# Optimization experiments

Measured on AMD Instinct MI355X. Metric: run time of the kernel, lower is better.

Reference implementation:

```python
import jax, jax.numpy as jnp
import numpy as np

B, S, D, H = 2, 2048, 2048, 16
HD = D // H


def setup_inputs() -> dict:
    key = jax.random.key(0)
    ks = jax.random.split(key, 9)
    scale = 0.02
    return {
        "x": jax.random.normal(ks[0], (B, S, D), dtype=jnp.float32),
        "wq_w": jax.random.normal(ks[1], (D, D), dtype=jnp.float32) * scale,
        "wq_b": jnp.zeros((D,), dtype=jnp.float32),
        "wk_w": jax.random.normal(ks[2], (D, D), dtype=jnp.float32) * scale,
        "wk_b": jnp.zeros((D,), dtype=jnp.float32),
        "wv_w": jax.random.normal(ks[3], (D, D), dtype=jnp.float32) * scale,
        "wv_b": jnp.zeros((D,), dtype=jnp.float32),
        "wo_w": jax.random.normal(ks[4], (D, D), dtype=jnp.float32) * scale,
        "wo_b": jnp.zeros((D,), dtype=jnp.float32),
    }


def reference(x, wq_w, wq_b, wk_w, wk_b, wv_w, wv_b, wo_w, wo_b):
    # torch Linear: y = x @ W.T + b
    q = x @ wq_w.T + wq_b  # [B,S,D]
    k = x @ wk_w.T + wk_b
    v = x @ wv_w.T + wv_b
    # [B,S,D] -> [B,H,S,HD]
    q = q.reshape(B, S, H, HD).transpose(0, 2, 1, 3)
    k = k.reshape(B, S, H, HD).transpose(0, 2, 1, 3)
    v = v.reshape(B, S, H, HD).transpose(0, 2, 1, 3)
    # scores [B,H,S,S], scaled by sqrt(d_dim) as in the original (not head_dim)
    scores = jnp.einsum("bhid,bhjd->bhij", q, k) / np.float32(np.sqrt(D))
    # faithful reproduction of the module's triu/transpose masking:
    m = jnp.swapaxes(jnp.triu(scores), -2, -1)  # lower-tri, zeros elsewhere
    p = jax.nn.softmax(m, axis=-2)              # softmax over dim=-2, zeros included
    a = jnp.swapaxes(jnp.triu(p), -2, -1)       # [B,H,S,S]
    attn = jnp.einsum("bhij,bhjd->bhid", a, v)  # [B,H,S,HD]
    concat = attn.transpose(0, 2, 1, 3).reshape(B, S, D)
    return concat @ wo_w.T + wo_b
```

## Files before the change

kernel.cpp:

```cpp
#include <hip/hip_runtime.h>

#define BB 2
#define SS 2048
#define DD 2048
#define HH 16
#define HDIM 128
#define MTOK (BB*SS)
#define BHH (BB*HH)
#define NCHUNK 16
#define QKN (2*DD)

typedef __attribute__((ext_vector_type(8))) __bf16 bf16x8;
typedef __attribute__((ext_vector_type(4))) float f32x4;
typedef __attribute__((ext_vector_type(8))) int i32x8;

__device__ __forceinline__ unsigned short f2bf(float f) {
  unsigned u = __float_as_uint(f);
  u += 0x7FFFu + ((u >> 16) & 1u);
  return (unsigned short)(u >> 16);
}
__device__ __forceinline__ float bf2f(unsigned short s) {
  return __uint_as_float(((unsigned)s) << 16);
}
__device__ __forceinline__ unsigned char f2e4m3(float f) {
  int pk = __builtin_amdgcn_cvt_pk_fp8_f32(f, f, 0, false);
  return (unsigned char)(pk & 0xFF);
}

#define GLOAD_LDS16(src, dst)                                                   \
  __builtin_amdgcn_global_load_lds(                                             \
      (const void __attribute__((address_space(1)))*)(src),                     \
      (void __attribute__((address_space(3)))*)(dst), 16, 0, 0)

__global__ void cvt_x_dual(const float* __restrict__ in,
                           unsigned short* __restrict__ outb,
                           unsigned int* __restrict__ out8, int n4) {
  int i = blockIdx.x * blockDim.x + threadIdx.x;
  if (i < n4) {
    float4 v = ((const float4*)in)[i];
    ushort4 o;
    o.x = f2bf(v.x); o.y = f2bf(v.y); o.z = f2bf(v.z); o.w = f2bf(v.w);
    ((ushort4*)outb)[i] = o;
    int p0 = __builtin_amdgcn_cvt_pk_fp8_f32(v.x, v.y, 0, false);
    int p1 = __builtin_amdgcn_cvt_pk_fp8_f32(v.z, v.w, 0, false);
    out8[i] = (unsigned)(p0 & 0xFFFF) | ((unsigned)(p1 & 0xFFFF) << 16);
  }
}

__global__ void cvt_wqk8(const float* __restrict__ a, const float* __restrict__ b,
                         unsigned int* __restrict__ out) {
  int i = blockIdx.x * blockDim.x + threadIdx.x;
  int sel = i >> 20, r = i & 0xFFFFF;
  const float* src = sel == 0 ? a : b;
  float4 v = ((const float4*)src)[r];
  int p0 = __builtin_amdgcn_cvt_pk_fp8_f32(v.x, v.y, 0, false);
  int p1 = __builtin_amdgcn_cvt_pk_fp8_f32(v.z, v.w, 0, false);
  out[i] = (unsigned)(p0 & 0xFFFF) | ((unsigned)(p1 & 0xFFFF) << 16);
}

__global__ void cvt_w2bf(const float* __restrict__ a, const float* __restrict__ b,
                         unsigned short* __restrict__ out) {
  int i = blockIdx.x * blockDim.x + threadIdx.x;
  int sel = i >> 20, r = i & 0xFFFFF;
  const float* src = sel == 0 ? a : b;
  float4 v = ((const float4*)src)[r];
  ushort4 o;
  o.x = f2bf(v.x); o.y = f2bf(v.y); o.z = f2bf(v.z); o.w = f2bf(v.w);
  ((ushort4*)out)[i] = o;
}

__global__ void concat2(const float* __restrict__ a, const float* __restrict__ b,
                        float* __restrict__ out) {
  int i = blockIdx.x * blockDim.x + threadIdx.x;
  if (i < DD) { out[i] = a[i]; out[DD + i] = b[i]; }
}

template <bool OUT_BF16>
__global__ __launch_bounds__(256, 2) void gemm_bt(
    const __bf16* __restrict__ A, const __bf16* __restrict__ W,
    const float* __restrict__ bias, void* __restrict__ Cout,
    int M, int N, int K) {
  __shared__ __bf16 lA[128 * 32];
  __shared__ __bf16 lB[128 * 32];
  const int t = threadIdx.x;
  const int lane = t & 63, wave = t >> 6;
  const int quad = lane >> 4, l16 = lane & 15;
  const int m0 = blockIdx.y * 128, n0 = blockIdx.x * 128;
  const int wm = (wave & 1) * 64, wn = (wave >> 1) * 64;

  f32x4 acc[4][4] = {};

  for (int k0 = 0; k0 < K; k0 += 32) {
#pragma unroll
    for (int c = 0; c < 2; ++c) {
      int lin = c * 256 + t;
      int row = lin >> 2;
      int col = (lin & 3) * 8;
      const __bf16* srcA = A + (size_t)(m0 + row) * K + k0 + col;
      const __bf16* srcB = W + (size_t)(n0 + row) * K + k0 + col;
      GLOAD_LDS16(srcA, &lA[(c * 256 + wave * 64) * 8]);
      GLOAD_LDS16(srcB, &lB[(c * 256 + wave * 64) * 8]);
    }
    __syncthreads();
    bf16x8 af[4], bfr[4];
#pragma unroll
    for (int mt = 0; mt < 4; ++mt)
      af[mt] = *(const bf16x8*)&lA[(wm + mt * 16 + l16) * 32 + quad * 8];
#pragma unroll
    for (int nt = 0; nt < 4; ++nt)
      bfr[nt] = *(const bf16x8*)&lB[(wn + nt * 16 + l16) * 32 + quad * 8];
#pragma unroll
    for (int mt = 0; mt < 4; ++mt)
#pragma unroll
      for (int nt = 0; nt < 4; ++nt)
        acc[mt][nt] = __builtin_amdgcn_mfma_f32_16x16x32_bf16(af[mt], bfr[nt],
                                                              acc[mt][nt], 0, 0, 0);
    __syncthreads();
  }

#pragma unroll
  for (int mt = 0; mt < 4; ++mt) {
#pragma unroll
    for (int nt = 0; nt < 4; ++nt) {
      int col = n0 + wn + nt * 16 + l16;
      float bv = bias[col];
#pragma unroll
      for (int r = 0; r < 4; ++r) {
        int row = m0 + wm + mt * 16 + quad * 4 + r;
        float v = acc[mt][nt][r] + bv;
        if constexpr (OUT_BF16)
          ((unsigned short*)Cout)[(size_t)row * N + col] = f2bf(v);
        else
          ((float*)Cout)[(size_t)row * N + col] = v;
      }
    }
  }
}

__global__ __launch_bounds__(256, 2) void gemm_qk_fp8(
    const unsigned char* __restrict__ A8, const unsigned char* __restrict__ W8,
    const float* __restrict__ bias, unsigned char* __restrict__ Cout,
    int M, int N, int K) {
  __shared__ unsigned char lA[128 * 128];
  __shared__ unsigned char lB[128 * 128];
  const int t = threadIdx.x;
  const int lane = t & 63, wave = t >> 6;
  const int quad = lane >> 4, l16 = lane & 15;
  const int m0 = blockIdx.y * 128, n0 = blockIdx.x * 128;
  const int wm = (wave & 1) * 64, wn = (wave >> 1) * 64;

  f32x4 acc[4][4] = {};

  for (int k0 = 0; k0 < K; k0 += 128) {
#pragma unroll
    for (int c = 0; c < 4; ++c) {
      int lin = c * 256 + t;
      int row = lin >> 3;
      int ch = lin & 7;
      const unsigned char* srcA = A8 + (size_t)(m0 + row) * K + k0 + ch * 16;
      const unsigned char* srcB = W8 + (size_t)(n0 + row) * K + k0 + ch * 16;
      GLOAD_LDS16(srcA, &lA[(c * 256 + wave * 64) * 16]);
      GLOAD_LDS16(srcB, &lB[(c * 256 + wave * 64) * 16]);
    }
    __syncthreads();
    i32x8 af[4];
#pragma unroll
    for (int mt = 0; mt < 4; ++mt)
      af[mt] = *(const i32x8*)&lA[(wm + mt * 16 + l16) * 128 + quad * 32];
#pragma unroll
    for (int nt = 0; nt < 4; ++nt) {
      i32x8 bfr = *(const i32x8*)&lB[(wn + nt * 16 + l16) * 128 + quad * 32];
#pragma unroll
      for (int mt = 0; mt < 4; ++mt)
        acc[mt][nt] = __builtin_amdgcn_mfma_scale_f32_16x16x128_f8f6f4(
            af[mt], bfr, acc[mt][nt], 0 , 0 ,
            0, 127 , 0, 127 );
    }
    __syncthreads();
  }

#pragma unroll
  for (int mt = 0; mt < 4; ++mt) {
#pragma unroll
    for (int nt = 0; nt < 4; ++nt) {
      int col = n0 + wn + nt * 16 + l16;
      float bv = bias[col];
#pragma unroll
      for (int r = 0; r < 4; ++r) {
        int row = m0 + wm + mt * 16 + quad * 4 + r;
        Cout[(size_t)row * N + col] = f2e4m3(acc[mt][nt][r] + bv);
      }
    }
  }
}

__global__ __launch_bounds__(256, 2) void qk_rowsum8(
    const unsigned char* __restrict__ q8, const unsigned char* __restrict__ k8,
    float* __restrict__ denom, float* __restrict__ diag) {
  __shared__ unsigned char lK[4 * 128 * 32];
  const int t = threadIdx.x;
  const int lane = t & 63, wave = t >> 6;
  const int quad = lane >> 4, l16 = lane & 15;
  const int bh = blockIdx.y;
  const int b = bh >> 4, h = bh & 15;
  const float scale = 0.02209708691207961f;

#pragma unroll
  for (int sub = 0; sub < 2; ++sub) {
    const int tile = (sub == 0) ? (int)blockIdx.x : 31 - (int)blockIdx.x;
    const int i0 = tile * 64;
    const int rowg = i0 + wave * 16;

    long long af[4];
    const unsigned char* qbase =
        q8 + (size_t)(b * SS + rowg + l16) * QKN + h * HDIM;
#pragma unroll
    for (int ks = 0; ks < 4; ++ks)
      af[ks] = *(const long long*)(qbase + ks * 32 + quad * 8);

    float rowsum[4] = {0.f, 0.f, 0.f, 0.f};
    float diagv[4] = {0.f, 0.f, 0.f, 0.f};

    for (int j0 = i0 & ~127; j0 < SS; j0 += 128) {
#pragma unroll
      for (int c = 0; c < 4; ++c) {
        int L = c * 256 + t;
        int ks = L >> 8;
        int rem = L & 255;
        int row = rem >> 1;
        int c2 = rem & 1;
        const unsigned char* src =
            k8 + (size_t)(b * SS + j0 + row) * QKN + h * HDIM + ks * 32 + c2 * 16;
        GLOAD_LDS16(src, &lK[(c * 256 + wave * 64) * 16]);
      }
      __syncthreads();
#pragma unroll
      for (int nt = 0; nt < 8; ++nt) {
        f32x4 acc = {0.f, 0.f, 0.f, 0.f};
#pragma unroll
        for (int ks = 0; ks < 4; ++ks) {
          long long bfr =
              *(const long long*)&lK[ks * 4096 + (nt * 16 + l16) * 32 + quad * 8];
          acc = __builtin_amdgcn_mfma_f32_16x16x32_fp8_fp8(af[ks], bfr, acc, 0, 0, 0);
        }
        int colg = j0 + nt * 16 + l16;
#pragma unroll
        for (int r = 0; r < 4; ++r) {
          int rg = rowg + quad * 4 + r;
          if (colg >= rg) {
            float e = __expf(acc[r] * scale);
            rowsum[r] += e;
            if (colg == rg) diagv[r] = e;
          }
        }
      }
      __syncthreads();
    }

#pragma unroll
    for (int r = 0; r < 4; ++r) {
      float s = rowsum[r], d = diagv[r];
#pragma unroll
      for (int off = 1; off < 16; off <<= 1) {
        s += __shfl_xor(s, off, 64);
        d += __shfl_xor(d, off, 64);
      }
      if (l16 == 0) {
        int rg = rowg + quad * 4 + r;
        denom[bh * SS + rg] = (float)rg + s;
        diag[bh * SS + rg] = d;
      }
    }
  }
}

__global__ void scan_pass1(const __bf16* __restrict__ v0,
                           float* __restrict__ csum) {
  int blk = blockIdx.x;
  int bh = blk >> 4, c = blk & 15;
  int b = bh >> 4, h = bh & 15;
  int t = threadIdx.x;
  int rs = t >> 4, dg = t & 15;
  const unsigned short* base = (const unsigned short*)v0 +
      (size_t)(b * SS + c * 128 + rs * 8) * DD + h * HDIM + dg * 8;
  float s[8] = {0.f, 0.f, 0.f, 0.f, 0.f, 0.f, 0.f, 0.f};
#pragma unroll
  for (int i = 0; i < 8; ++i) {
    uint4 u = *(const uint4*)(base + (size_t)i * DD);
    const unsigned short* us = (const unsigned short*)&u;
#pragma unroll
    for (int j = 0; j < 8; ++j) s[j] += bf2f(us[j]);
  }
  __shared__ float red[16 * 128];
#pragma unroll
  for (int j = 0; j < 8; ++j) red[rs * 128 + dg * 8 + j] = s[j];
  __syncthreads();
  for (int st = 8; st >= 1; st >>= 1) {
    if (rs < st) {
#pragma unroll
      for (int j = 0; j < 8; ++j)
        red[rs * 128 + dg * 8 + j] += red[(rs + st) * 128 + dg * 8 + j];
    }
    __syncthreads();
  }
  if (rs == 0) {
#pragma unroll
    for (int j = 0; j < 8; ++j)
      csum[(size_t)blk * 128 + dg * 8 + j] = red[dg * 8 + j];
  }
}

__global__ void scan_pass2(const __bf16* __restrict__ v0,
                           const float* __restrict__ csum,
                           const float* __restrict__ denom,
                           const float* __restrict__ diag,
                           unsigned short* __restrict__ ctx) {
  int blk = blockIdx.x;
  int bh = blk >> 4, c = blk & 15;
  int b = bh >> 4, h = bh & 15;
  int t = threadIdx.x;
  int rs = t >> 4, dg = t & 15;
  const unsigned short* vbase = (const unsigned short*)v0 +
      (size_t)(b * SS + c * 128 + rs * 8) * DD + h * HDIM + dg * 8;
  float vrow[8][8];
  float ls[8] = {0.f, 0.f, 0.f, 0.f, 0.f, 0.f, 0.f, 0.f};
#pragma unroll
  for (int i = 0; i < 8; ++i) {
    uint4 u = *(const uint4*)(vbase + (size_t)i * DD);
    const unsigned short* us = (const unsigned short*)&u;
#pragma unroll
    for (int j = 0; j < 8; ++j) {
      vrow[i][j] = bf2f(us[j]);
      ls[j] += vrow[i][j];
    }
  }
  __shared__ float red[16 * 128];
#pragma unroll
  for (int j = 0; j < 8; ++j) red[rs * 128 + dg * 8 + j] = ls[j];
  __syncthreads();

  float pre[8] = {0.f, 0.f, 0.f, 0.f, 0.f, 0.f, 0.f, 0.f};
  for (int cc = 0; cc < c; ++cc) {
    const float* cp = csum + (size_t)(bh * 16 + cc) * 128 + dg * 8;
#pragma unroll
    for (int j = 0; j < 8; ++j) pre[j] += cp[j];
  }
  for (int ss2 = 0; ss2 < rs; ++ss2) {
#pragma unroll
    for (int j = 0; j < 8; ++j) pre[j] += red[ss2 * 128 + dg * 8 + j];
  }

  int row0 = c * 128 + rs * 8;
  unsigned short* obase =
      ctx + (size_t)(b * SS + row0) * DD + h * HDIM + dg * 8;
  const float* dn = denom + bh * SS + row0;
  const float* dgp = diag + bh * SS + row0;
#pragma unroll
  for (int i = 0; i < 8; ++i) {
    float inv = 1.0f / dn[i];
    float dv = dgp[i];
    unsigned short o[8];
#pragma unroll
    for (int j = 0; j < 8; ++j) {
      float val = (pre[j] + dv * vrow[i][j]) * inv;
      o[j] = f2bf(val);
      pre[j] += vrow[i][j];
    }
    *(uint4*)(obase + (size_t)i * DD) = *(const uint4*)o;
  }
}

extern "C" void kernel_launch(void* const* d_in, const int* in_sizes, int n_in,
                              void* d_out, int out_size, void* d_ws, size_t ws_size,
                              hipStream_t stream) {
  (void)in_sizes; (void)n_in; (void)out_size; (void)ws_size;
  const float* x    = (const float*)d_in[0];
  const float* wq_w = (const float*)d_in[1];
  const float* wq_b = (const float*)d_in[2];
  const float* wk_w = (const float*)d_in[3];
  const float* wk_b = (const float*)d_in[4];
  const float* wv_w = (const float*)d_in[5];
  const float* wv_b = (const float*)d_in[6];
  const float* wo_w = (const float*)d_in[7];
  const float* wo_b = (const float*)d_in[8];

  char* ws = (char*)d_ws;
  size_t off = 0;
  auto alloc = [&](size_t bytes) {
    char* p = ws + off;
    off += (bytes + 255) & ~(size_t)255;
    return p;
  };
  unsigned short* xb   = (unsigned short*)alloc((size_t)MTOK * DD * 2);
  unsigned char*  x8   = (unsigned char*)alloc((size_t)MTOK * DD);
  unsigned char*  wqk8 = (unsigned char*)alloc((size_t)2 * DD * DD);
  unsigned short* wvo  = (unsigned short*)alloc((size_t)2 * DD * DD * 2);
  unsigned char*  qk8  = (unsigned char*)alloc((size_t)MTOK * QKN);
  unsigned short* v    = (unsigned short*)alloc((size_t)MTOK * DD * 2);
  unsigned short* ctx  = (unsigned short*)alloc((size_t)MTOK * DD * 2);
  float* biasqk = (float*)alloc((size_t)2 * DD * 4);
  float* denom  = (float*)alloc((size_t)BHH * SS * 4);
  float* diag   = (float*)alloc((size_t)BHH * SS * 4);
  float* csum   = (float*)alloc((size_t)BHH * NCHUNK * 128 * 4);

  {
    int n4 = MTOK * DD / 4;
    cvt_x_dual<<<n4 / 256, 256, 0, stream>>>(x, xb, (unsigned int*)x8, n4);
    cvt_wqk8<<<(2 << 20) / 256, 256, 0, stream>>>(wq_w, wk_w, (unsigned int*)wqk8);
    cvt_w2bf<<<(2 << 20) / 256, 256, 0, stream>>>(wv_w, wo_w, wvo);
    concat2<<<(DD + 255) / 256, 256, 0, stream>>>(wq_b, wk_b, biasqk);
  }

  gemm_qk_fp8<<<dim3(QKN / 128, MTOK / 128), 256, 0, stream>>>(
      x8, wqk8, biasqk, qk8, MTOK, QKN, DD);

  gemm_bt<true><<<dim3(DD / 128, MTOK / 128), 256, 0, stream>>>(
      (const __bf16*)xb, (const __bf16*)wvo, wv_b, v, MTOK, DD, DD);

  qk_rowsum8<<<dim3(16, BHH), 256, 0, stream>>>(
      qk8,
      qk8 + DD,
      denom, diag);

  scan_pass1<<<BHH * NCHUNK, 256, 0, stream>>>((const __bf16*)v, csum);
  scan_pass2<<<BHH * NCHUNK, 256, 0, stream>>>((const __bf16*)v, csum,
                                               denom, diag, ctx);

  gemm_bt<false><<<dim3(DD / 128, MTOK / 128), 256, 0, stream>>>(
      (const __bf16*)ctx, (const __bf16*)(wvo + (size_t)DD * DD), wo_b,
      d_out, MTOK, DD, DD);
}
```

Before: 367.8 us.

## Rework QK rowsum kernel with K=128 MFMA, double buffering, split-K halves, swizzled LDS

The QK row-sum kernel now uses the 16x16x128 scaled FP8 MFMA over 64-row tiles per block, double-buffers the K tiles in LDS, and splits the column range across two blocks. The two partial denominators are written to separate buffers and added in scan_pass2. Causal masking is applied only on the first diagonal tile, and exp is computed with exp2 and a folded constant. Both the QK GEMM and the rowsum kernel use an XOR swizzle on their LDS layouts to reduce bank conflicts. In exchange the kernel uses more LDS and registers, and the launch-bounds occupancy hint is raised.

```diff
diff --git a/kernel.cpp b/kernel.cpp
--- a/kernel.cpp
+++ b/kernel.cpp
@@ -13,6 +13,7 @@
 typedef __attribute__((ext_vector_type(8))) __bf16 bf16x8;
 typedef __attribute__((ext_vector_type(4))) float f32x4;
 typedef __attribute__((ext_vector_type(8))) int i32x8;
+typedef __attribute__((ext_vector_type(4))) int i32x4;
 
 __device__ __forceinline__ unsigned short f2bf(float f) {
   unsigned u = __float_as_uint(f);
@@ -148,6 +149,7 @@
   const int quad = lane >> 4, l16 = lane & 15;
   const int m0 = blockIdx.y * 128, n0 = blockIdx.x * 128;
   const int wm = (wave & 1) * 64, wn = (wave >> 1) * 64;
+  const int p0 = (2 * quad) ^ (l16 & 7);
 
   f32x4 acc[4][4] = {};
 
@@ -157,19 +159,26 @@
       int lin = c * 256 + t;
       int row = lin >> 3;
       int ch = lin & 7;
-      const unsigned char* srcA = A8 + (size_t)(m0 + row) * K + k0 + ch * 16;
-      const unsigned char* srcB = W8 + (size_t)(n0 + row) * K + k0 + ch * 16;
+      int sch = ch ^ (row & 7);
+      const unsigned char* srcA = A8 + (size_t)(m0 + row) * K + k0 + sch * 16;
+      const unsigned char* srcB = W8 + (size_t)(n0 + row) * K + k0 + sch * 16;
       GLOAD_LDS16(srcA, &lA[(c * 256 + wave * 64) * 16]);
       GLOAD_LDS16(srcB, &lB[(c * 256 + wave * 64) * 16]);
     }
     __syncthreads();
     i32x8 af[4];
 #pragma unroll
-    for (int mt = 0; mt < 4; ++mt)
-      af[mt] = *(const i32x8*)&lA[(wm + mt * 16 + l16) * 128 + quad * 32];
+    for (int mt = 0; mt < 4; ++mt) {
+      int ra = (wm + mt * 16 + l16) * 128 + p0 * 16;
+      ((i32x4*)&af[mt])[0] = *(const i32x4*)&lA[ra];
+      ((i32x4*)&af[mt])[1] = *(const i32x4*)&lA[ra ^ 16];
+    }
 #pragma unroll
     for (int nt = 0; nt < 4; ++nt) {
-      i32x8 bfr = *(const i32x8*)&lB[(wn + nt * 16 + l16) * 128 + quad * 32];
+      int rb = (wn + nt * 16 + l16) * 128 + p0 * 16;
+      i32x8 bfr;
+      ((i32x4*)&bfr)[0] = *(const i32x4*)&lB[rb];
+      ((i32x4*)&bfr)[1] = *(const i32x4*)&lB[rb ^ 16];
 #pragma unroll
       for (int mt = 0; mt < 4; ++mt)
         acc[mt][nt] = __builtin_amdgcn_mfma_scale_f32_16x16x128_f8f6f4(
@@ -194,81 +203,151 @@
   }
 }
 
-__global__ __launch_bounds__(256, 2) void qk_rowsum8(
+__global__ __launch_bounds__(256, 4) void qk_rowsum8(
     const unsigned char* __restrict__ q8, const unsigned char* __restrict__ k8,
-    float* __restrict__ denom, float* __restrict__ diag) {
-  __shared__ unsigned char lK[4 * 128 * 32];
+    float* __restrict__ denomA, float* __restrict__ denomB,
+    float* __restrict__ diag) {
+  __shared__ unsigned char lK[2][128 * 128];
+  __shared__ float redS[4][64];
+  __shared__ float redD[4][64];
   const int t = threadIdx.x;
   const int lane = t & 63, wave = t >> 6;
   const int quad = lane >> 4, l16 = lane & 15;
   const int bh = blockIdx.y;
   const int b = bh >> 4, h = bh & 15;
-  const float scale = 0.02209708691207961f;
-
-#pragma unroll
+  const int pair = blockIdx.x >> 1;
+  const int half = blockIdx.x & 1;
+  const float C = 0.03187935771f;
+  const f32x4 fz = {0.f, 0.f, 0.f, 0.f};
+
+  int soff[4];
+#pragma unroll
+  for (int c = 0; c < 4; ++c) {
+    int L = c * 256 + t;
+    int row = L >> 3, p = L & 7;
+    soff[c] = row * QKN + ((p ^ (row & 7)) * 16);
+  }
+  const int p0 = (2 * quad) ^ (l16 & 7);
+  int bo[2];
+#pragma unroll
+  for (int nt = 0; nt < 2; ++nt)
+    bo[nt] = (wave * 32 + nt * 16 + l16) * 128 + p0 * 16;
+
+  const unsigned char* kbase = k8 + (size_t)(b * SS) * QKN + h * HDIM;
+
   for (int sub = 0; sub < 2; ++sub) {
-    const int tile = (sub == 0) ? (int)blockIdx.x : 31 - (int)blockIdx.x;
+    const int tile = (sub == 0) ? pair : 31 - pair;
     const int i0 = tile * 64;
-    const int rowg = i0 + wave * 16;
-
-    long long af[4];
-    const unsigned char* qbase =
-        q8 + (size_t)(b * SS + rowg + l16) * QKN + h * HDIM;
-#pragma unroll
-    for (int ks = 0; ks < 4; ++ks)
-      af[ks] = *(const long long*)(qbase + ks * 32 + quad * 8);
-
-    float rowsum[4] = {0.f, 0.f, 0.f, 0.f};
-    float diagv[4] = {0.f, 0.f, 0.f, 0.f};
-
-    for (int j0 = i0 & ~127; j0 < SS; j0 += 128) {
-#pragma unroll
-      for (int c = 0; c < 4; ++c) {
-        int L = c * 256 + t;
-        int ks = L >> 8;
-        int rem = L & 255;
-        int row = rem >> 1;
-        int c2 = rem & 1;
-        const unsigned char* src =
-            k8 + (size_t)(b * SS + j0 + row) * QKN + h * HDIM + ks * 32 + c2 * 16;
-        GLOAD_LDS16(src, &lK[(c * 256 + wave * 64) * 16]);
+    const int jbase = i0 & ~127;
+    const int ntile = (SS - jbase) >> 7;
+
+    i32x8 af[4];
+    {
+      const unsigned char* qbase =
+          q8 + (size_t)(b * SS + i0 + l16) * QKN + h * HDIM + quad * 32;
+#pragma unroll
+      for (int mt = 0; mt < 4; ++mt)
+        af[mt] = *(const i32x8*)(qbase + (size_t)(mt * 16) * QKN);
+    }
+
+    float rowacc[4][4] = {};
+
+    int kidx = half;
+    if (kidx < ntile) {
+      {
+        const unsigned char* src = kbase + (size_t)(jbase + kidx * 128) * QKN;
+#pragma unroll
+        for (int c = 0; c < 4; ++c)
+          GLOAD_LDS16(src + soff[c], &lK[0][(c * 256 + wave * 64) * 16]);
       }
+      asm volatile("s_waitcnt vmcnt(0)" ::: "memory");
       __syncthreads();
-#pragma unroll
-      for (int nt = 0; nt < 8; ++nt) {
-        f32x4 acc = {0.f, 0.f, 0.f, 0.f};
-#pragma unroll
-        for (int ks = 0; ks < 4; ++ks) {
-          long long bfr =
-              *(const long long*)&lK[ks * 4096 + (nt * 16 + l16) * 32 + quad * 8];
-          acc = __builtin_amdgcn_mfma_f32_16x16x32_fp8_fp8(af[ks], bfr, acc, 0, 0, 0);
+      int cur = 0;
+      for (; kidx < ntile; kidx += 2, cur ^= 1) {
+        if (kidx + 2 < ntile) {
+          const unsigned char* src =
+              kbase + (size_t)(jbase + (kidx + 2) * 128) * QKN;
+#pragma unroll
+          for (int c = 0; c < 4; ++c)
+            GLOAD_LDS16(src + soff[c], &lK[cur ^ 1][(c * 256 + wave * 64) * 16]);
         }
-        int colg = j0 + nt * 16 + l16;
-#pragma unroll
-        for (int r = 0; r < 4; ++r) {
-          int rg = rowg + quad * 4 + r;
-          if (colg >= rg) {
-            float e = __expf(acc[r] * scale);
-            rowsum[r] += e;
-            if (colg == rg) diagv[r] = e;
+        const unsigned char* lkc = lK[cur];
+        const int j0 = jbase + kidx * 128;
+        if (kidx == 0) {
+          float dloc[4][4] = {};
+#pragma unroll
+          for (int nt = 0; nt < 2; ++nt) {
+            i32x8 bf;
+            ((i32x4*)&bf)[0] = *(const i32x4*)(lkc + bo[nt]);
+            ((i32x4*)&bf)[1] = *(const i32x4*)(lkc + (bo[nt] ^ 16));
+            f32x4 acc[4];
+#pragma unroll
+            for (int mt = 0; mt < 4; ++mt)
+              acc[mt] = __builtin_amdgcn_mfma_scale_f32_16x16x128_f8f6f4(
+                  af[mt], bf, fz, 0, 0, 0, 127, 0, 127);
+            const int colg = j0 + wave * 32 + nt * 16 + l16;
+#pragma unroll
+            for (int mt = 0; mt < 4; ++mt)
+#pragma unroll
+              for (int r = 0; r < 4; ++r) {
+                int rg = i0 + mt * 16 + quad * 4 + r;
+                float e = (colg >= rg)
+                              ? __builtin_amdgcn_exp2f(acc[mt][r] * C) : 0.f;
+                rowacc[mt][r] += e;
+                if (colg == rg) dloc[mt][r] = e;
+              }
+          }
+#pragma unroll
+          for (int mt = 0; mt < 4; ++mt)
+#pragma unroll
+            for (int r = 0; r < 4; ++r) {
+              float d = dloc[mt][r];
+#pragma unroll
+              for (int off = 1; off < 16; off <<= 1) d += __shfl_xor(d, off, 64);
+              if (l16 == 0) redD[wave][mt * 16 + quad * 4 + r] = d;
+            }
+        } else {
+#pragma unroll
+          for (int nt = 0; nt < 2; ++nt) {
+            i32x8 bf;
+            ((i32x4*)&bf)[0] = *(const i32x4*)(lkc + bo[nt]);
+            ((i32x4*)&bf)[1] = *(const i32x4*)(lkc + (bo[nt] ^ 16));
+            f32x4 acc[4];
+#pragma unroll
+            for (int mt = 0; mt < 4; ++mt)
+              acc[mt] = __builtin_amdgcn_mfma_scale_f32_16x16x128_f8f6f4(
+                  af[mt], bf, fz, 0, 0, 0, 127, 0, 127);
+#pragma unroll
+            for (int mt = 0; mt < 4; ++mt)
+#pragma unroll
+              for (int r = 0; r < 4; ++r)
+                rowacc[mt][r] += __builtin_amdgcn_exp2f(acc[mt][r] * C);
           }
         }
+        asm volatile("s_waitcnt vmcnt(0)" ::: "memory");
+        __syncthreads();
       }
-      __syncthreads();
-    }
-
-#pragma unroll
-    for (int r = 0; r < 4; ++r) {
-      float s = rowsum[r], d = diagv[r];
-#pragma unroll
-      for (int off = 1; off < 16; off <<= 1) {
-        s += __shfl_xor(s, off, 64);
-        d += __shfl_xor(d, off, 64);
+    }
+
+    __syncthreads();
+#pragma unroll
+    for (int mt = 0; mt < 4; ++mt)
+#pragma unroll
+      for (int r = 0; r < 4; ++r) {
+        float s = rowacc[mt][r];
+#pragma unroll
+        for (int off = 1; off < 16; off <<= 1) s += __shfl_xor(s, off, 64);
+        if (l16 == 0) redS[wave][mt * 16 + quad * 4 + r] = s;
       }
-      if (l16 == 0) {
-        int rg = rowg + quad * 4 + r;
-        denom[bh * SS + rg] = (float)rg + s;
-        diag[bh * SS + rg] = d;
+    __syncthreads();
+    if (t < 64) {
+      const int rg = i0 + t;
+      float s = redS[0][t] + redS[1][t] + redS[2][t] + redS[3][t];
+      if (half == 0) {
+        denomA[bh * SS + rg] = (float)rg + s;
+        diag[bh * SS + rg] = redD[0][t] + redD[1][t] + redD[2][t] + redD[3][t];
+      } else {
+        denomB[bh * SS + rg] = s;
       }
     }
   }
@@ -312,7 +391,8 @@
 
 __global__ void scan_pass2(const __bf16* __restrict__ v0,
                            const float* __restrict__ csum,
-                           const float* __restrict__ denom,
+                           const float* __restrict__ denomA,
+                           const float* __restrict__ denomB,
                            const float* __restrict__ diag,
                            unsigned short* __restrict__ ctx) {
   int blk = blockIdx.x;
@@ -353,11 +433,12 @@
   int row0 = c * 128 + rs * 8;
   unsigned short* obase =
       ctx + (size_t)(b * SS + row0) * DD + h * HDIM + dg * 8;
-  const float* dn = denom + bh * SS + row0;
+  const float* dnA = denomA + bh * SS + row0;
+  const float* dnB = denomB + bh * SS + row0;
   const float* dgp = diag + bh * SS + row0;
 #pragma unroll
   for (int i = 0; i < 8; ++i) {
-    float inv = 1.0f / dn[i];
+    float inv = 1.0f / (dnA[i] + dnB[i]);
     float dv = dgp[i];
     unsigned short o[8];
 #pragma unroll
@@ -399,7 +480,8 @@
   unsigned short* v    = (unsigned short*)alloc((size_t)MTOK * DD * 2);
   unsigned short* ctx  = (unsigned short*)alloc((size_t)MTOK * DD * 2);
   float* biasqk = (float*)alloc((size_t)2 * DD * 4);
-  float* denom  = (float*)alloc((size_t)BHH * SS * 4);
+  float* denomA = (float*)alloc((size_t)BHH * SS * 4);
+  float* denomB = (float*)alloc((size_t)BHH * SS * 4);
   float* diag   = (float*)alloc((size_t)BHH * SS * 4);
   float* csum   = (float*)alloc((size_t)BHH * NCHUNK * 128 * 4);
 
@@ -417,14 +499,14 @@
   gemm_bt<true><<<dim3(DD / 128, MTOK / 128), 256, 0, stream>>>(
       (const __bf16*)xb, (const __bf16*)wvo, wv_b, v, MTOK, DD, DD);
 
-  qk_rowsum8<<<dim3(16, BHH), 256, 0, stream>>>(
+  qk_rowsum8<<<dim3(32, BHH), 256, 0, stream>>>(
       qk8,
       qk8 + DD,
-      denom, diag);
+      denomA, denomB, diag);
 
   scan_pass1<<<BHH * NCHUNK, 256, 0, stream>>>((const __bf16*)v, csum);
   scan_pass2<<<BHH * NCHUNK, 256, 0, stream>>>((const __bf16*)v, csum,
-                                               denom, diag, ctx);
+                                               denomA, denomB, diag, ctx);
 
   gemm_bt<false><<<dim3(DD / 128, MTOK / 128), 256, 0, stream>>>(
       (const __bf16*)ctx, (const __bf16*)(wvo + (size_t)DD * DD), wo_b,
```

Measured after the change: 349.4 us. 5.0% less time.
